# Performance work log

Hardware: AMD Instinct MI355X
Metric: run time of the kernel (lower is better)

The kernel has to match this reference:

```python
import jax, jax.numpy as jnp
import numpy as np

DIMS, K_SIZE, V_SIZE, SEQ_LEN = 1024, 128, 128, 2048
MINUS = -100.0


def setup_inputs() -> dict:
    key = jax.random.key(0)
    k1, k2, k3, k4, k5 = jax.random.split(key, 5)
    B, S = 8, 2048
    minibatch = jax.random.normal(k1, (B, S, DIMS), dtype=jnp.float32)
    # Linear params (torch nn.Linear default init scale ~ U(-1/sqrt(fan_in), ...)); use scaled normals
    s = 1.0 / np.sqrt(DIMS)
    Wk = jax.random.normal(k2, (DIMS, K_SIZE), dtype=jnp.float32) * s
    bk = jax.random.normal(k3, (K_SIZE,), dtype=jnp.float32) * s
    Wv = jax.random.normal(k4, (DIMS, V_SIZE), dtype=jnp.float32) * s
    bv = jax.random.normal(k5, (V_SIZE,), dtype=jnp.float32) * s
    return {"minibatch": minibatch, "Wk": Wk, "bk": bk, "Wv": Wv, "bv": bv,
            "current_seq_len": S}


def reference(minibatch, Wk, bk, Wv, bv, current_seq_len):
    # keys == queries (shared projection, as in the original forward)
    keys = minibatch @ Wk + bk              # [B,S,K]
    values = minibatch @ Wv + bv            # [B,S,V]
    S = current_seq_len
    mask = jnp.tril(jnp.ones((S, S), dtype=jnp.float32))  # [S,S] lower-triangular
    scores = jnp.einsum('bsk,btk->bst', keys, keys) / np.sqrt(K_SIZE)
    logits = mask * scores + MINUS * (1.0 - mask)
    probs = jax.nn.softmax(logits, axis=2)
    read = jnp.einsum('bst,btv->bsv', probs, values)  # [B,S,V]
    return jnp.concatenate([minibatch, read], axis=2)  # [B,S,dims+V]
```

## Files before the change

### kernel.cpp

```cpp
#include <hip/hip_runtime.h>
#include <hip/hip_bf16.h>

#define BATCH 8
#define SEQ   2048
#define DMS   1024
#define KSZ   128
#define OD    1152

typedef unsigned short u16;
typedef unsigned int   u32;
typedef __attribute__((ext_vector_type(4)))  float  f32x4;
typedef __attribute__((ext_vector_type(16))) float  f32x16;
typedef __attribute__((ext_vector_type(8)))  __bf16 bf16x8;

union U128 { uint4 u4; bf16x8 b8; u16 us[8]; u32 u[4]; };

__device__ inline u16 f2bf(float f) {
  union { __bf16 h; u16 u; } c;
  c.h = (__bf16)f;
  return c.u;
}

__device__ inline u32 packbf2(float a, float b) {
  return (u32)f2bf(a) | ((u32)f2bf(b) << 16);
}

__device__ inline float fexp2(float x) {
  float r;
  asm("v_exp_f32 %0, %1" : "=v"(r) : "v"(x));
  return r;
}

__device__ inline f32x16 mfma32(bf16x8 a, bf16x8 b, f32x16 c) {
  return __builtin_amdgcn_mfma_f32_32x32x16_bf16(a, b, c, 0, 0, 0);
}

__device__ inline uint4 pack8bf(float4 a, float4 b) {
  U128 w;
  w.us[0] = f2bf(a.x); w.us[1] = f2bf(a.y);
  w.us[2] = f2bf(a.z); w.us[3] = f2bf(a.w);
  w.us[4] = f2bf(b.x); w.us[5] = f2bf(b.y);
  w.us[6] = f2bf(b.z); w.us[7] = f2bf(b.w);
  return w.u4;
}

#define BSTRIDE 262144


__global__ void __launch_bounds__(256) prep_kernel(
    const float* __restrict__ Wk, const float* __restrict__ Wv,
    u16* __restrict__ Wfrag)
{
  int T = blockIdx.x * 256 + threadIdx.x;
  int lane = T & 63;
  int fragid = T >> 6;
  int ks = fragid >> 3, cf = fragid & 7;
  int l31 = lane & 31, hi = lane >> 5;
  int n = cf * 32 + l31;
  const float* src = (n < 128) ? (Wk + n) : (Wv + (n - 128));
  int k0 = ks * 16 + hi * 8;
  U128 w;
#pragma unroll
  for (int j = 0; j < 8; ++j) w.us[j] = f2bf(src[(size_t)(k0 + j) * KSZ]);
  *(uint4*)(Wfrag + (size_t)T * 8) = w.u4;
}

__global__ void __launch_bounds__(512, 1) gemm_kernel(
    const float* __restrict__ X, const u16* __restrict__ Wfrag,
    const float* __restrict__ bk, const float* __restrict__ bv,
    u16* __restrict__ Kfrag, u16* __restrict__ Vfrag)
{
  __shared__ u16 Xl[64 * 1024];

  const int tid  = threadIdx.x;
  const int lane = tid & 63;
  const int w    = tid >> 6;
  const int rh   = w >> 2;
  const int cq   = w & 3;
  const int l31  = lane & 31;
  const int hi   = lane >> 5;
  const int m0   = blockIdx.x * 64;

  {
    const int u  = tid & 127;
    const int ro = tid >> 7;
#pragma unroll
    for (int h = 0; h < 4; ++h) {
      float4 t0[4], t1[4];
#pragma unroll
      for (int p = 0; p < 4; ++p) {
        int row = h * 16 + p * 4 + ro;
        const float4* xp = (const float4*)(X + (size_t)(m0 + row) * DMS + u * 8);
        t0[p] = xp[0]; t1[p] = xp[1];
      }
#pragma unroll
      for (int p = 0; p < 4; ++p) {
        int row = h * 16 + p * 4 + ro;
        *(uint4*)(Xl + row * 1024 + ((u * 8) ^ ((row & 7) << 3))) =
            pack8bf(t0[p], t1[p]);
      }
    }
  }
  __syncthreads();

  f32x16 a0, a1;
#pragma unroll
  for (int i = 0; i < 16; ++i) { a0[i] = 0.f; a1[i] = 0.f; }

  const u16* wb = Wfrag + (size_t)(cq * 2) * 512 + hi * 256 + l31 * 8;
  const int xrow  = rh * 32 + l31;
  const int xbase = xrow * 1024;
  const int xswz  = (xrow & 7) << 3;

#pragma unroll 4
  for (int ks = 0; ks < 64; ++ks) {
    U128 xa;
    xa.u4 = *(const uint4*)(Xl + xbase + ((ks * 16 + hi * 8) ^ xswz));
    U128 w0, w1;
    const u16* wp = wb + (size_t)ks * 4096;
    w0.u4 = *(const uint4*)(wp);
    w1.u4 = *(const uint4*)(wp + 512);
    if (cq < 2) {
      a0 = mfma32(w0.b8, xa.b8, a0);
      a1 = mfma32(w1.b8, xa.b8, a1);
    } else {
      a0 = mfma32(xa.b8, w0.b8, a0);
      a1 = mfma32(xa.b8, w1.b8, a1);
    }
  }

  const int bb = m0 >> 11;
  const int t2 = ((m0 & 2047) >> 5) + rh;

  if (cq < 2) {
#pragma unroll
    for (int r = 0; r < 16; ++r) {
      int crow = (r & 3) + 8 * (r >> 2) + 4 * hi;
      a0[r] += bk[cq * 64 + crow];
      a1[r] += bk[cq * 64 + 32 + crow];
    }
    u16* kb = Kfrag + (size_t)bb * BSTRIDE + (size_t)(t2 * 8) * 512 + l31 * 8;
#pragma unroll
    for (int ct = 0; ct < 2; ++ct) {
      const f32x16 a = ct ? a1 : a0;
      u32 c0 = packbf2(a[0],  a[1]),  c1 = packbf2(a[2],  a[3]);
      u32 c2 = packbf2(a[4],  a[5]),  c3 = packbf2(a[6],  a[7]);
      u32 c4 = packbf2(a[8],  a[9]),  c5 = packbf2(a[10], a[11]);
      u32 c6 = packbf2(a[12], a[13]), c7 = packbf2(a[14], a[15]);
      u32 d0 = __shfl_xor(c0, 32), d1 = __shfl_xor(c1, 32);
      u32 d2 = __shfl_xor(c2, 32), d3 = __shfl_xor(c3, 32);
      u32 d4 = __shfl_xor(c4, 32), d5 = __shfl_xor(c5, 32);
      u32 d6 = __shfl_xor(c6, 32), d7 = __shfl_xor(c7, 32);
      int ks2 = cq * 4 + ct * 2 + hi;
      uint4 rA, rB;
      if (hi == 0) {
        rA = (uint4){c0, c1, d0, d1};
        rB = (uint4){c2, c3, d2, d3};
      } else {
        rA = (uint4){d4, d5, c4, c5};
        rB = (uint4){d6, d7, c6, c7};
      }
      *(uint4*)(kb + (size_t)ks2 * 512)       = rA;
      *(uint4*)(kb + (size_t)ks2 * 512 + 256) = rB;
    }
  } else {
    const int vq = cq - 2;
#pragma unroll
    for (int ct = 0; ct < 2; ++ct) {
      float bvv = bv[vq * 64 + ct * 32 + l31];
      if (ct) { for (int r = 0; r < 16; ++r) a1[r] += bvv; }
      else    { for (int r = 0; r < 16; ++r) a0[r] += bvv; }
    }
    u16* vb = Vfrag + (size_t)bb * BSTRIDE + l31 * 8;
#pragma unroll
    for (int ct = 0; ct < 2; ++ct) {
      const f32x16 a = ct ? a1 : a0;
      u32 c0 = packbf2(a[0],  a[1]),  c1 = packbf2(a[2],  a[3]);
      u32 c2 = packbf2(a[4],  a[5]),  c3 = packbf2(a[6],  a[7]);
      u32 c4 = packbf2(a[8],  a[9]),  c5 = packbf2(a[10], a[11]);
      u32 c6 = packbf2(a[12], a[13]), c7 = packbf2(a[14], a[15]);
      u32 d0 = __shfl_xor(c0, 32), d1 = __shfl_xor(c1, 32);
      u32 d2 = __shfl_xor(c2, 32), d3 = __shfl_xor(c3, 32);
      u32 d4 = __shfl_xor(c4, 32), d5 = __shfl_xor(c5, 32);
      u32 d6 = __shfl_xor(c6, 32), d7 = __shfl_xor(c7, 32);
      int vb2 = vq * 2 + ct;
      int th  = hi;
      uint4 rA, rB;
      if (hi == 0) {
        rA = (uint4){c0, c1, d0, d1};
        rB = (uint4){c2, c3, d2, d3};
      } else {
        rA = (uint4){d4, d5, c4, c5};
        rB = (uint4){d6, d7, c6, c7};
      }
      u16* dst = vb + (size_t)((t2 * 4 + vb2) * 2 + th) * 512;
      *(uint4*)(dst)       = rA;
      *(uint4*)(dst + 256) = rB;
    }
  }
}

__global__ void __launch_bounds__(256, 2) attn_kernel(
    const u16* __restrict__ Kfrag, const u16* __restrict__ Vfrag,
    const float* __restrict__ X, float* __restrict__ out)
{
  __shared__ float Om[4][128][33];
  __shared__ float Ml[4][2][32];
  __shared__ float Wm[4][32];
  __shared__ float Li[32];

  const int tid  = threadIdx.x;
  const int lane = tid & 63;
  const int w    = tid >> 6;
  const int l31  = lane & 31;
  const int hi   = lane >> 5;

  const int bi = blockIdx.x;
  const int b  = bi & 7;
  const int qt = (bi < 256) ? (63 - (bi >> 3)) : ((bi >> 3) - 32);
  const int q0 = qt * 32;

  const u16* Kb = Kfrag + (size_t)b * BSTRIDE;
  const u16* Vb = Vfrag + (size_t)b * BSTRIDE;
  const int loff = hi * 256 + l31 * 8;

  bf16x8 qf[8];
  {
    const u16* qp = Kb + (size_t)(qt * 8) * 512 + loff;
#pragma unroll
    for (int ks = 0; ks < 8; ++ks) {
      U128 u; u.u4 = *(const uint4*)(qp + ks * 512); qf[ks] = u.b8;
    }
  }

  f32x16 o[4];
#pragma unroll
  for (int vb2 = 0; vb2 < 4; ++vb2)
#pragma unroll
    for (int i = 0; i < 16; ++i) o[vb2][i] = 0.f;

  float mrun = -3.0e38f, lsum = 0.f;
  const float SC  = 0.08838834764831845f;
  const float L2E = 1.44269504088896341f;

  bf16x8 kf[8];
  {
    int ti0 = (w <= qt) ? w : 0;
    const u16* kp = Kb + (size_t)(ti0 * 8) * 512 + loff;
#pragma unroll
    for (int ks = 0; ks < 8; ++ks) {
      U128 u; u.u4 = *(const uint4*)(kp + ks * 512); kf[ks] = u.b8;
    }
  }

  for (int ti = w; ti <= qt; ti += 4) {
    bf16x8 vf[4][2];
    {
      const u16* vp = Vb + (size_t)(ti * 8) * 512 + loff;
#pragma unroll
      for (int vb2 = 0; vb2 < 4; ++vb2)
#pragma unroll
        for (int th = 0; th < 2; ++th) {
          U128 u; u.u4 = *(const uint4*)(vp + (vb2 * 2 + th) * 512);
          vf[vb2][th] = u.b8;
        }
    }
    f32x16 s;
#pragma unroll
    for (int i = 0; i < 16; ++i) s[i] = 0.f;
#pragma unroll
    for (int ks = 0; ks < 8; ++ks) s = mfma32(kf[ks], qf[ks], s);
    {
      int tin = (ti + 4 <= qt) ? ti + 4 : ti;
      const u16* kp = Kb + (size_t)(tin * 8) * 512 + loff;
#pragma unroll
      for (int ks = 0; ks < 8; ++ks) {
        U128 u; u.u4 = *(const uint4*)(kp + ks * 512); kf[ks] = u.b8;
      }
    }
    float sv[16];
#pragma unroll
    for (int r = 0; r < 16; ++r) sv[r] = s[r] * SC;
    if (ti == qt) {
#pragma unroll
      for (int r = 0; r < 16; ++r) {
        int toff = (r & 3) + 8 * (r >> 2) + 4 * hi;
        if (toff > l31) sv[r] = -3.0e38f;
      }
    }
    float mx = sv[0];
#pragma unroll
    for (int r = 1; r < 16; ++r) mx = fmaxf(mx, sv[r]);
    mx = fmaxf(mx, __shfl_xor(mx, 32));
    float p[16];
    float ps = 0.f;
    if (__all(mx - mrun <= 8.0f)) {
#pragma unroll
      for (int r = 0; r < 16; ++r) { p[r] = fexp2((sv[r] - mrun) * L2E); ps += p[r]; }
      ps += __shfl_xor(ps, 32);
      lsum += ps;
    } else {
      float mnew = fmaxf(mrun, mx);
      float al = fexp2((mrun - mnew) * L2E);
#pragma unroll
      for (int r = 0; r < 16; ++r) { p[r] = fexp2((sv[r] - mnew) * L2E); ps += p[r]; }
      ps += __shfl_xor(ps, 32);
      lsum = lsum * al + ps;
      mrun = mnew;
#pragma unroll
      for (int vb2 = 0; vb2 < 4; ++vb2)
#pragma unroll
        for (int i = 0; i < 16; ++i) o[vb2][i] *= al;
    }
    u32 c01 = packbf2(p[0],  p[1]);
    u32 c23 = packbf2(p[2],  p[3]);
    u32 c45 = packbf2(p[4],  p[5]);
    u32 c67 = packbf2(p[6],  p[7]);
    u32 c89 = packbf2(p[8],  p[9]);
    u32 cAB = packbf2(p[10], p[11]);
    u32 cCD = packbf2(p[12], p[13]);
    u32 cEF = packbf2(p[14], p[15]);
    u32 d01 = __shfl_xor(c01, 32);
    u32 d23 = __shfl_xor(c23, 32);
    u32 d45 = __shfl_xor(c45, 32);
    u32 d67 = __shfl_xor(c67, 32);
    u32 d89 = __shfl_xor(c89, 32);
    u32 dAB = __shfl_xor(cAB, 32);
    u32 dCD = __shfl_xor(cCD, 32);
    u32 dEF = __shfl_xor(cEF, 32);
    U128 pf1, pf2;
    pf1.u[0] = hi ? d45 : c01;
    pf1.u[1] = hi ? d67 : c23;
    pf1.u[2] = hi ? c45 : d01;
    pf1.u[3] = hi ? c67 : d23;
    pf2.u[0] = hi ? dCD : c89;
    pf2.u[1] = hi ? dEF : cAB;
    pf2.u[2] = hi ? cCD : d89;
    pf2.u[3] = hi ? cEF : dAB;
#pragma unroll
    for (int vb2 = 0; vb2 < 4; ++vb2) {
      o[vb2] = mfma32(vf[vb2][0], pf1.b8, o[vb2]);
      o[vb2] = mfma32(vf[vb2][1], pf2.b8, o[vb2]);
    }
  }

#pragma unroll
  for (int vb2 = 0; vb2 < 4; ++vb2)
#pragma unroll
    for (int r = 0; r < 16; ++r) {
      int v = vb2 * 32 + (r & 3) + 8 * (r >> 2) + 4 * hi;
      Om[w][v][l31] = o[vb2][r];
    }
  if (lane < 32) {
    Ml[w][0][l31] = mrun;
    Ml[w][1][l31] = lsum;
  }
  __syncthreads();

  if (tid < 32) {
    float m0 = Ml[0][0][tid], m1 = Ml[1][0][tid];
    float m2 = Ml[2][0][tid], m3 = Ml[3][0][tid];
    float M  = fmaxf(fmaxf(m0, m1), fmaxf(m2, m3));
    float w0 = fexp2((m0 - M) * L2E), w1 = fexp2((m1 - M) * L2E);
    float w2 = fexp2((m2 - M) * L2E), w3 = fexp2((m3 - M) * L2E);
    float L  = Ml[0][1][tid] * w0 + Ml[1][1][tid] * w1 +
               Ml[2][1][tid] * w2 + Ml[3][1][tid] * w3;
    Wm[0][tid] = w0; Wm[1][tid] = w1; Wm[2][tid] = w2; Wm[3][tid] = w3;
    Li[tid] = 1.f / L;
  }
  __syncthreads();

  {
    const int q = tid >> 3;
    const int vbase = (tid & 7) * 16;
    float wq0 = Wm[0][q], wq1 = Wm[1][q], wq2 = Wm[2][q], wq3 = Wm[3][q];
    float li = Li[q];
    float* orow = out + (size_t)(b * SEQ + q0 + q) * OD + 1024 + vbase;
#pragma unroll
    for (int i = 0; i < 16; i += 4) {
      float4 res;
      res.x = (Om[0][vbase + i + 0][q] * wq0 + Om[1][vbase + i + 0][q] * wq1 +
               Om[2][vbase + i + 0][q] * wq2 + Om[3][vbase + i + 0][q] * wq3) * li;
      res.y = (Om[0][vbase + i + 1][q] * wq0 + Om[1][vbase + i + 1][q] * wq1 +
               Om[2][vbase + i + 1][q] * wq2 + Om[3][vbase + i + 1][q] * wq3) * li;
      res.z = (Om[0][vbase + i + 2][q] * wq0 + Om[1][vbase + i + 2][q] * wq1 +
               Om[2][vbase + i + 2][q] * wq2 + Om[3][vbase + i + 2][q] * wq3) * li;
      res.w = (Om[0][vbase + i + 3][q] * wq0 + Om[1][vbase + i + 3][q] * wq1 +
               Om[2][vbase + i + 3][q] * wq2 + Om[3][vbase + i + 3][q] * wq3) * li;
      *(float4*)(orow + i) = res;
    }
  }

  {
#pragma unroll
    for (int r0 = 0; r0 < 32; r0 += 8) {
      float4 t[8];
#pragma unroll
      for (int j = 0; j < 8; ++j)
        t[j] = *((const float4*)(X + (size_t)(b * SEQ + q0 + r0 + j) * DMS) + tid);
#pragma unroll
      for (int j = 0; j < 8; ++j)
        *((float4*)(out + (size_t)(b * SEQ + q0 + r0 + j) * OD) + tid) = t[j];
    }
  }
}

extern "C" void kernel_launch(void* const* d_in, const int* in_sizes, int n_in,
                              void* d_out, int out_size, void* d_ws, size_t ws_size,
                              hipStream_t stream)
{
  const float* X  = (const float*)d_in[0];
  const float* Wk = (const float*)d_in[1];
  const float* bk = (const float*)d_in[2];
  const float* Wv = (const float*)d_in[3];
  const float* bv = (const float*)d_in[4];
  float* out = (float*)d_out;

  u16* Kfrag = (u16*)d_ws;
  u16* Vfrag = Kfrag + (size_t)BATCH * BSTRIDE;
  u16* Wfrag = Vfrag + (size_t)BATCH * BSTRIDE;

  prep_kernel<<<dim3(128), dim3(256), 0, stream>>>(Wk, Wv, Wfrag);
  gemm_kernel<<<dim3(256), dim3(512), 0, stream>>>(X, Wfrag, bk, bv, Kfrag, Vfrag);
  attn_kernel<<<dim3(512), dim3(256), 0, stream>>>(Kfrag, Vfrag, X, out);
}
```

Baseline: 73.65 us.

## Copy X passthrough into output inside GEMM and halve GEMM tile

```diff
diff --git a/kernel.cpp b/kernel.cpp
--- a/kernel.cpp
+++ b/kernel.cpp
@@ -65,21 +65,19 @@
   *(uint4*)(Wfrag + (size_t)T * 8) = w.u4;
 }
 
-__global__ void __launch_bounds__(512, 1) gemm_kernel(
+__global__ void __launch_bounds__(256, 2) gemm_kernel(
     const float* __restrict__ X, const u16* __restrict__ Wfrag,
     const float* __restrict__ bk, const float* __restrict__ bv,
-    u16* __restrict__ Kfrag, u16* __restrict__ Vfrag)
+    float* __restrict__ out, u16* __restrict__ Kfrag, u16* __restrict__ Vfrag)
 {
-  __shared__ u16 Xl[64 * 1024];
+  __shared__ u16 Xl[32 * 1024];
 
   const int tid  = threadIdx.x;
   const int lane = tid & 63;
-  const int w    = tid >> 6;
-  const int rh   = w >> 2;
-  const int cq   = w & 3;
+  const int cq   = tid >> 6;
   const int l31  = lane & 31;
   const int hi   = lane >> 5;
-  const int m0   = blockIdx.x * 64;
+  const int m0   = blockIdx.x * 32;
 
   {
     const int u  = tid & 127;
@@ -89,13 +87,16 @@
       float4 t0[4], t1[4];
 #pragma unroll
       for (int p = 0; p < 4; ++p) {
-        int row = h * 16 + p * 4 + ro;
+        int row = (h * 4 + p) * 2 + ro;
         const float4* xp = (const float4*)(X + (size_t)(m0 + row) * DMS + u * 8);
         t0[p] = xp[0]; t1[p] = xp[1];
       }
 #pragma unroll
       for (int p = 0; p < 4; ++p) {
-        int row = h * 16 + p * 4 + ro;
+        int row = (h * 4 + p) * 2 + ro;
+        float* op = out + (size_t)(m0 + row) * OD + u * 8;
+        *(float4*)op = t0[p];
+        *(float4*)(op + 4) = t1[p];
         *(uint4*)(Xl + row * 1024 + ((u * 8) ^ ((row & 7) << 3))) =
             pack8bf(t0[p], t1[p]);
       }
@@ -108,9 +109,8 @@
   for (int i = 0; i < 16; ++i) { a0[i] = 0.f; a1[i] = 0.f; }
 
   const u16* wb = Wfrag + (size_t)(cq * 2) * 512 + hi * 256 + l31 * 8;
-  const int xrow  = rh * 32 + l31;
-  const int xbase = xrow * 1024;
-  const int xswz  = (xrow & 7) << 3;
+  const int xbase = l31 * 1024;
+  const int xswz  = (l31 & 7) << 3;
 
 #pragma unroll 4
   for (int ks = 0; ks < 64; ++ks) {
@@ -130,7 +130,7 @@
   }
 
   const int bb = m0 >> 11;
-  const int t2 = ((m0 & 2047) >> 5) + rh;
+  const int t2 = (m0 & 2047) >> 5;
 
   if (cq < 2) {
 #pragma unroll
@@ -202,7 +202,7 @@
 
 __global__ void __launch_bounds__(256, 2) attn_kernel(
     const u16* __restrict__ Kfrag, const u16* __restrict__ Vfrag,
-    const float* __restrict__ X, float* __restrict__ out)
+    float* __restrict__ out)
 {
   __shared__ float Om[4][128][33];
   __shared__ float Ml[4][2][32];
@@ -390,19 +390,6 @@
       *(float4*)(orow + i) = res;
     }
   }
-
-  {
-#pragma unroll
-    for (int r0 = 0; r0 < 32; r0 += 8) {
-      float4 t[8];
-#pragma unroll
-      for (int j = 0; j < 8; ++j)
-        t[j] = *((const float4*)(X + (size_t)(b * SEQ + q0 + r0 + j) * DMS) + tid);
-#pragma unroll
-      for (int j = 0; j < 8; ++j)
-        *((float4*)(out + (size_t)(b * SEQ + q0 + r0 + j) * OD) + tid) = t[j];
-    }
-  }
 }
 
 extern "C" void kernel_launch(void* const* d_in, const int* in_sizes, int n_in,
@@ -421,6 +408,6 @@
   u16* Wfrag = Vfrag + (size_t)BATCH * BSTRIDE;
 
   prep_kernel<<<dim3(128), dim3(256), 0, stream>>>(Wk, Wv, Wfrag);
-  gemm_kernel<<<dim3(256), dim3(512), 0, stream>>>(X, Wfrag, bk, bv, Kfrag, Vfrag);
-  attn_kernel<<<dim3(512), dim3(256), 0, stream>>>(Kfrag, Vfrag, X, out);
-}
+  gemm_kernel<<<dim3(512), dim3(256), 0, stream>>>(X, Wfrag, bk, bv, out, Kfrag, Vfrag);
+  attn_kernel<<<dim3(512), dim3(256), 0, stream>>>(Kfrag, Vfrag, out);
+}
```

Result: no change. 74.82 us (+1.6%).
